# Kernel optimization log

Hardware: AMD Instinct MI355X
Metric: run time of the kernel (lower is better)

Reference implementation:

```python
import jax, jax.numpy as jnp
import numpy as np

D_MODEL = 1024
D_INNER = 4096
K = 127
B, L = 2, 4096

def setup_inputs() -> dict:
    key = jax.random.key(0)
    k1, k2, k3, k4, k5 = jax.random.split(key, 5)
    x = jax.random.normal(k1, (B, L, D_MODEL), dtype=jnp.float32)
    # in_proj: Linear(d, 2*m) -> weight [2m, d] (torch convention)
    w_in = jax.random.normal(k2, (2 * D_INNER, D_MODEL), dtype=jnp.float32) * (1.0 / np.sqrt(D_MODEL))
    # depthwise conv weight: [m, 1, k] in torch; store as [m, k]
    w_dw = jax.random.normal(k3, (D_INNER, K), dtype=jnp.float32) * (1.0 / np.sqrt(K))
    b_dw = jax.random.normal(k4, (D_INNER,), dtype=jnp.float32) * 0.01
    # out_proj: Linear(m, d) -> weight [d, m]
    w_out = jax.random.normal(k5, (D_MODEL, D_INNER), dtype=jnp.float32) * (1.0 / np.sqrt(D_INNER))
    return {"x": x, "w_in": w_in, "w_dw": w_dw, "b_dw": b_dw, "w_out": w_out}

def _causal_dwconv(v, w_dw, b_dw):
    # v: [B, L, m]; causal depthwise conv with kernel K
    # pad K-1 on the left only (equivalent to torch pad=K-1 then [..., :L])
    v_bcl = jnp.transpose(v, (0, 2, 1))  # [B, m, L]
    out = jax.lax.conv_general_dilated(
        v_bcl,
        w_dw[:, None, :],  # [m, 1, K]
        window_strides=(1,),
        padding=[(K - 1, 0)],
        feature_group_count=D_INNER,
        dimension_numbers=("NCH", "OIH", "NCH"),
    )
    out = out + b_dw[None, :, None]
    return jnp.transpose(out, (0, 2, 1))  # [B, L, m]

def reference(x, w_in, w_dw, b_dw, w_out):
    vg = jnp.einsum("bld,ed->ble", x, w_in)  # [B, L, 2m]
    v, g = jnp.split(vg, 2, axis=-1)
    v = _causal_dwconv(v, w_dw, b_dw)
    y = jax.nn.silu(v) * jax.nn.silu(g)
    return jnp.einsum("blm,dm->bld", y, w_out)
```

## Files before the change

### kernel.cpp

```cpp
#include <hip/hip_runtime.h>
#include <hip/hip_bf16.h>
#include <cstdint>
#include <cstddef>

typedef __fp16 f16_t;
typedef __attribute__((ext_vector_type(8))) __fp16 f16x8;
typedef __attribute__((ext_vector_type(4))) __fp16 f16x4;
typedef __attribute__((ext_vector_type(2))) __fp16 h2_t;
typedef __attribute__((ext_vector_type(4))) float floatx4;

__device__ __forceinline__ void async_copy_16B(const void* g, void* l) {
  __builtin_amdgcn_global_load_lds(
      (const __attribute__((address_space(1))) void*)g,
      (__attribute__((address_space(3))) void*)l, 16, 0, 0);
}

#define ISSUE_FENCE asm volatile("" ::: "memory")

__global__ __launch_bounds__(256) void prep(
    const float* __restrict__ x, const float* __restrict__ w_in,
    const float* __restrict__ w_out, const float* __restrict__ w_dw,
    f16_t* __restrict__ x_h, f16_t* __restrict__ wi_h,
    f16_t* __restrict__ wo_h, h2_t* __restrict__ wp) {
  const int tid = blockIdx.x * 256 + threadIdx.x;
  if (tid < 5242880) {
    const float* src;
    f16_t* dst;
    int off;
    if (tid < 2097152) {
      src = x; dst = x_h; off = tid;
    } else if (tid < 4194304) {
      src = w_in; dst = wi_h; off = tid - 2097152;
    } else {
      src = w_out; dst = wo_h; off = tid - 4194304;
    }
    const float4 v = *(const float4*)(src + (size_t)off * 4);
    f16x4 o;
    o.x = (f16_t)v.x; o.y = (f16_t)v.y; o.z = (f16_t)v.z; o.w = (f16_t)v.w;
    *(f16x4*)(dst + (size_t)off * 4) = o;
  } else {
    const int idx = tid - 5242880;
    if (idx < 128 * 4096) {
      const int p = idx >> 12;
      const int c = idx & 4095;
      float a, b;
      if (p < 126) {
        a = w_dw[c * 127 + p]; b = w_dw[c * 127 + p + 1];
      } else if (p == 126) {
        a = w_dw[c * 127 + 126]; b = 0.f;
      } else {
        a = 0.f; b = w_dw[c * 127 + 0];
      }
      h2_t w;
      w.x = (f16_t)a; w.y = (f16_t)b;
      wp[idx] = w;
    }
  }
}

__global__ __launch_bounds__(512, 2) void gemm256_8p(
    const f16_t* __restrict__ A, const f16_t* __restrict__ B,
    f16_t* __restrict__ C, int M, int N, int K) {
  extern __shared__ char smem[];
  const int t = threadIdx.x;
  const int lane = t & 63;
  const int wave = t >> 6;
  const int wm = wave >> 2;
  const int wn = wave & 3;

  const int bid = blockIdx.x;
  const int swz = (bid & 7) * 128 + (bid >> 3);
  const int m0 = (swz >> 5) * 256;
  const int n0 = (swz & 31) * 256;

  const int fr = lane & 15;
  const int ks = lane >> 4;

  auto stageB = [&](int d, int k0, int half) {
#pragma unroll
    for (int l = 0; l < 2; ++l) {
      const int q = l * 512 + t;
      const int row = half * 128 + (q >> 3);
      const int slot = q & 7;
      const int col = (slot ^ (row & 7)) * 8;
      async_copy_16B(B + (size_t)(n0 + row) * K + k0 + col,
                     smem + d * 65536 + 32768 + row * 128 + slot * 16);
    }
  };
  auto stageA = [&](int d, int k0, int j) {
    const int blk = t >> 8;
    const int row = j * 32 + blk * 128 + ((t & 255) >> 3);
    const int slot = t & 7;
    const int col = (slot ^ (row & 7)) * 8;
    async_copy_16B(A + (size_t)(m0 + row) * K + k0 + col,
                   smem + d * 65536 + row * 128 + slot * 16);
  };
  auto ldA = [&](int d, int R, int kslot) -> f16x8 {
    return *(const f16x8*)(smem + d * 65536 + R * 128 +
                           ((kslot ^ (R & 7)) << 4));
  };
  auto ldB = [&](int d, int R, int kslot) -> f16x8 {
    return *(const f16x8*)(smem + d * 65536 + 32768 + R * 128 +
                           ((kslot ^ (R & 7)) << 4));
  };

  floatx4 acc[8][4] = {};
  const int kTiles = K / 64;

  stageB(0, 0, 0); ISSUE_FENCE;
  stageB(0, 0, 1); ISSUE_FENCE;
  stageA(0, 0, 0); ISSUE_FENCE;
  stageA(0, 0, 1); ISSUE_FENCE;
  stageA(0, 0, 2); ISSUE_FENCE;
  stageA(0, 0, 3); ISSUE_FENCE;
  asm volatile("s_waitcnt vmcnt(3)" ::: "memory");
  __builtin_amdgcn_s_barrier();

  f16x8 bf[4][2];
  for (int tt = 0; tt < kTiles; ++tt) {
    const int d = tt & 1;
    const int kn = (tt + 1) * 64;
    const bool pf = (tt + 1 < kTiles);
#pragma unroll
    for (int q = 0; q < 4; ++q) {
      f16x8 af[2][2];
#pragma unroll
      for (int kh = 0; kh < 2; ++kh) {
#pragma unroll
        for (int ii = 0; ii < 2; ++ii)
          af[ii][kh] = ldA(d, wm * 128 + q * 32 + ii * 16 + fr, kh * 4 + ks);
        if (q == 0)
#pragma unroll
          for (int j = 0; j < 4; ++j)
            bf[j][kh] = ldB(d, wn * 64 + j * 16 + fr, kh * 4 + ks);
      }
      if (pf) {
        if (q == 0) stageB(d ^ 1, kn, 0);
        else if (q == 1) stageB(d ^ 1, kn, 1);
        else if (q == 2) { stageA(d ^ 1, kn, 0); stageA(d ^ 1, kn, 1); }
        else { stageA(d ^ 1, kn, 2); stageA(d ^ 1, kn, 3); }
      }
      if (pf) {
        if (q == 0)      asm volatile("s_waitcnt vmcnt(4)" ::: "memory");
        else if (q == 1) asm volatile("s_waitcnt vmcnt(5)" ::: "memory");
        else if (q == 2) asm volatile("s_waitcnt vmcnt(6)" ::: "memory");
        else             asm volatile("s_waitcnt vmcnt(3)" ::: "memory");
      } else {
        if (q == 0)      asm volatile("s_waitcnt vmcnt(2)" ::: "memory");
        else if (q == 1) asm volatile("s_waitcnt vmcnt(1)" ::: "memory");
        else if (q == 2) asm volatile("s_waitcnt vmcnt(0)" ::: "memory");
      }
      __builtin_amdgcn_s_barrier();
      __builtin_amdgcn_s_setprio(1);
#pragma unroll
      for (int kh = 0; kh < 2; ++kh)
#pragma unroll
        for (int ii = 0; ii < 2; ++ii)
#pragma unroll
          for (int j = 0; j < 4; ++j)
            acc[q * 2 + ii][j] = __builtin_amdgcn_mfma_f32_16x16x32_f16(
                af[ii][kh], bf[j][kh], acc[q * 2 + ii][j], 0, 0, 0);
      __builtin_amdgcn_s_setprio(0);
      __builtin_amdgcn_s_barrier();
    }
  }

  const int cr = (lane >> 4) * 4;
  const int cc = lane & 15;
#pragma unroll
  for (int i = 0; i < 8; ++i)
#pragma unroll
    for (int j = 0; j < 4; ++j)
#pragma unroll
      for (int r = 0; r < 4; ++r) {
        const int row = m0 + wm * 128 + i * 16 + cr + r;
        const int col = n0 + wn * 64 + j * 16 + cc;
        C[(size_t)row * N + col] = (f16_t)acc[i][j][r];
      }
}

__global__ __launch_bounds__(256) void gemm_bt_k128(
    const f16_t* __restrict__ A, const f16_t* __restrict__ B,
    float* __restrict__ C, int M, int N, int K) {
  constexpr int BM_ = 128, BN_ = 64, KP = 4;
  constexpr int NA = BM_ * 4 * KP;
  constexpr int NTOT = (BM_ + BN_) * 4 * KP;
  constexpr int CPT = NTOT / 256;

  __shared__ f16_t smem[(BM_ + BN_) * 128];
  const int t = threadIdx.x;
  const int lane = t & 63;
  const int wave = t >> 6;
  const int m0 = blockIdx.y * BM_;
  const int n0 = blockIdx.x * BN_;
  const int wr = wave * 32;
  const int fr = lane & 15;
  const int fk = (lane >> 4) * 8;

  floatx4 acc[2][4] = {};

  const int kTiles = K / 128;
  for (int kt = 0; kt < kTiles; ++kt) {
    const int k0 = kt * 128;
    __syncthreads();
#pragma unroll
    for (int it = 0; it < CPT; ++it) {
      const int p = it * 256 + t;
      const f16_t* gsrc;
      if (p < NA) {
        const int h = p >> 9;
        const int r = (p >> 2) & (BM_ - 1);
        const int kc = h * 32 + (p & 3) * 8;
        gsrc = A + (size_t)(m0 + r) * K + k0 + kc;
      } else {
        const int q = p - NA;
        const int h = q >> 8;
        const int r = (q >> 2) & (BN_ - 1);
        const int kc = h * 32 + (q & 3) * 8;
        gsrc = B + (size_t)(n0 + r) * K + k0 + kc;
      }
      async_copy_16B(gsrc, smem + p * 8);
    }
    __syncthreads();

#pragma unroll
    for (int h = 0; h < KP; ++h) {
      f16x8 af[2], bf[4];
#pragma unroll
      for (int i = 0; i < 2; ++i)
        af[i] = *(const f16x8*)(smem + h * BM_ * 32 + (wr + i * 16 + fr) * 32 + fk);
#pragma unroll
      for (int j = 0; j < 4; ++j)
        bf[j] = *(const f16x8*)(smem + NA * 8 + h * BN_ * 32 + (j * 16 + fr) * 32 + fk);
#pragma unroll
      for (int i = 0; i < 2; ++i)
#pragma unroll
        for (int j = 0; j < 4; ++j)
          acc[i][j] = __builtin_amdgcn_mfma_f32_16x16x32_f16(
              af[i], bf[j], acc[i][j], 0, 0, 0);
    }
  }

  const int cr = (lane >> 4) * 4;
  const int cc = lane & 15;
#pragma unroll
  for (int i = 0; i < 2; ++i)
#pragma unroll
    for (int j = 0; j < 4; ++j)
#pragma unroll
      for (int r = 0; r < 4; ++r) {
        const int row = m0 + wr + i * 16 + cr + r;
        const int col = n0 + j * 16 + cc;
        C[(size_t)row * N + col] = acc[i][j][r];
      }
}

#define CONV_L 128
#define CPAIRS 127

__global__ __launch_bounds__(256) void conv_gate(
    const f16_t* __restrict__ vg, const h2_t* __restrict__ wp,
    const float* __restrict__ b_dw, f16_t* __restrict__ y) {
  __shared__ uint32_t vtp[CPAIRS * 64];
  __shared__ uint32_t wpl[128 * 64];
  const int t = threadIdx.x;
  const int lane = t & 63;
  const int wave = t >> 6;
  const int c0 = blockIdx.x * 64;
  const int lt = blockIdx.y & 31;
  const int b = blockIdx.y >> 5;
  const int l0 = lt * CONV_L;

#pragma unroll
  for (int it = 0; it < 8; ++it) {
    const int q = it * 256 + t;
    async_copy_16B(wp + (size_t)(q >> 4) * 4096 + c0 + (q & 15) * 4,
                   wpl + q * 4);
  }
  for (int q = t; q < CPAIRS * 8; q += 256) {
    const int m = q >> 3;
    const int oc = (q & 7) * 8;
    const int le = l0 - 126 + 2 * m;
    uint4 a = make_uint4(0u, 0u, 0u, 0u);
    uint4 bb = make_uint4(0u, 0u, 0u, 0u);
    if (le >= 0) {
      const size_t base = (size_t)(b * 4096 + le) * 8192 + c0 + oc;
      a = *(const uint4*)(vg + base);
      bb = *(const uint4*)(vg + base + 8192);
    }
    uint32_t* dst = vtp + m * 64 + oc;
    const uint32_t aw[4] = {a.x, a.y, a.z, a.w};
    const uint32_t bw[4] = {bb.x, bb.y, bb.z, bb.w};
#pragma unroll
    for (int i = 0; i < 4; ++i) {
      dst[2 * i] = (aw[i] & 0xFFFFu) | (bw[i] << 16);
      dst[2 * i + 1] = (aw[i] >> 16) | (bw[i] & 0xFFFF0000u);
    }
  }

  const int c = c0 + lane;
  const int lb = l0 + wave * 32;
  const f16_t* gp = vg + (size_t)(b * 4096 + lb) * 8192 + 4096 + c;
  f16_t gvals[32];
#pragma unroll
  for (int i = 0; i < 32; ++i) gvals[i] = gp[(size_t)i * 8192];

  __syncthreads();

  const float bias = b_dw[c];
  float acc[32];
#pragma unroll
  for (int i = 0; i < 32; ++i) acc[i] = bias;

  const uint32_t* vbase = vtp + wave * 16 * 64 + lane;
  const uint32_t* wbase = wpl + lane;

  h2_t ring[17];
#pragma unroll
  for (int m = 0; m < 17; ++m)
    ring[m] = __builtin_bit_cast(h2_t, vbase[m * 64]);

  {
    const h2_t w0 = __builtin_bit_cast(h2_t, wbase[127 * 64]);
#pragma unroll
    for (int h = 0; h < 16; ++h)
      acc[2 * h + 1] =
          __builtin_amdgcn_fdot2(w0, ring[h], acc[2 * h + 1], false);
  }

#pragma unroll
  for (int k = 0; k < 64; ++k) {
    const h2_t we = __builtin_bit_cast(h2_t, wbase[(2 * k) * 64]);
#pragma unroll
    for (int h = 0; h < 16; ++h)
      acc[2 * h] =
          __builtin_amdgcn_fdot2(we, ring[(k + h) % 17], acc[2 * h], false);
    if (k < 63) {
      const h2_t wo = __builtin_bit_cast(h2_t, wbase[(2 * k + 1) * 64]);
#pragma unroll
      for (int h = 0; h < 16; ++h)
        acc[2 * h + 1] = __builtin_amdgcn_fdot2(wo, ring[(k + 1 + h) % 17],
                                                acc[2 * h + 1], false);
      if (k < 62)
        ring[k % 17] = __builtin_bit_cast(h2_t, vbase[(17 + k) * 64]);
    }
  }

  f16_t* yp = y + (size_t)(b * 4096 + lb) * 4096 + c;
#pragma unroll
  for (int i = 0; i < 32; ++i) {
    const float gv = (float)gvals[i];
    const float v = acc[i];
    const float sv = v / (1.f + __expf(-v));
    const float sg = gv / (1.f + __expf(-gv));
    yp[(size_t)i * 4096] = (f16_t)(sv * sg);
  }
}

extern "C" void kernel_launch(void* const* d_in, const int* in_sizes, int n_in,
                              void* d_out, int out_size, void* d_ws,
                              size_t ws_size, hipStream_t stream) {
  const float* x     = (const float*)d_in[0];
  const float* w_in  = (const float*)d_in[1];
  const float* w_dw  = (const float*)d_in[2];
  const float* b_dw  = (const float*)d_in[3];
  const float* w_out = (const float*)d_in[4];
  float* out = (float*)d_out;

  char* p = (char*)d_ws;
  f16_t* x_h  = (f16_t*)p; p += (size_t)8192 * 1024 * 2;
  f16_t* wi_h = (f16_t*)p; p += (size_t)8192 * 1024 * 2;
  f16_t* wo_h = (f16_t*)p; p += (size_t)1024 * 4096 * 2;
  h2_t*  wp   = (h2_t*)p;  p += (size_t)128 * 4096 * 4;
  f16_t* vg   = (f16_t*)p; p += (size_t)8192 * 8192 * 2;
  f16_t* y    = (f16_t*)p; p += (size_t)8192 * 4096 * 2;

  prep<<<22528, 256, 0, stream>>>(x, w_in, w_out, w_dw, x_h, wi_h, wo_h, wp);

  hipFuncSetAttribute(reinterpret_cast<const void*>(gemm256_8p),
                      hipFuncAttributeMaxDynamicSharedMemorySize, 131072);
  gemm256_8p<<<1024, 512, 131072, stream>>>(x_h, wi_h, vg, 8192, 8192, 1024);

  conv_gate<<<dim3(64, 64), 256, 0, stream>>>(vg, wp, b_dw, y);
  gemm_bt_k128<<<dim3(16, 64), 256, 0, stream>>>(y, wo_h, out,
                                                 8192, 1024, 4096);
}
```

Baseline: 502.6 us.

## Deepen GEMM prefetch to two tiles ahead and remap blocks per XCD

```diff
diff --git a/kernel.cpp b/kernel.cpp
--- a/kernel.cpp
+++ b/kernel.cpp
@@ -14,8 +14,6 @@
       (const __attribute__((address_space(1))) void*)g,
       (__attribute__((address_space(3))) void*)l, 16, 0, 0);
 }
-
-#define ISSUE_FENCE asm volatile("" ::: "memory")
 
 __global__ __launch_bounds__(256) void prep(
     const float* __restrict__ x, const float* __restrict__ w_in,
@@ -69,17 +67,21 @@
   const int wn = wave & 3;
 
   const int bid = blockIdx.x;
-  const int swz = (bid & 7) * 128 + (bid >> 3);
-  const int m0 = (swz >> 5) * 256;
-  const int n0 = (swz & 31) * 256;
+  const int xcd = bid & 7;
+  const int l = bid >> 3;
+  const int quad = l >> 5;
+  const int qm = (l >> 3) & 3;
+  const int qn = l & 7;
+  const int m0 = ((xcd >> 1) * 8 + (quad >> 1) * 4 + qm) * 256;
+  const int n0 = ((xcd & 1) * 16 + (quad & 1) * 8 + qn) * 256;
 
   const int fr = lane & 15;
   const int ks = lane >> 4;
 
   auto stageB = [&](int d, int k0, int half) {
 #pragma unroll
-    for (int l = 0; l < 2; ++l) {
-      const int q = l * 512 + t;
+    for (int u = 0; u < 2; ++u) {
+      const int q = u * 512 + t;
       const int row = half * 128 + (q >> 3);
       const int slot = q & 7;
       const int col = (slot ^ (row & 7)) * 8;
@@ -107,20 +109,21 @@
   floatx4 acc[8][4] = {};
   const int kTiles = K / 64;
 
-  stageB(0, 0, 0); ISSUE_FENCE;
-  stageB(0, 0, 1); ISSUE_FENCE;
-  stageA(0, 0, 0); ISSUE_FENCE;
-  stageA(0, 0, 1); ISSUE_FENCE;
-  stageA(0, 0, 2); ISSUE_FENCE;
-  stageA(0, 0, 3); ISSUE_FENCE;
-  asm volatile("s_waitcnt vmcnt(3)" ::: "memory");
+  stageB(0, 0, 0); stageB(0, 0, 1);
+  stageA(0, 0, 0); stageA(0, 0, 1); stageA(0, 0, 2); stageA(0, 0, 3);
+  stageB(1, 64, 0); stageA(1, 64, 0);
+  stageB(1, 64, 1); stageA(1, 64, 1);
+  stageA(1, 64, 2);
+  asm volatile("s_waitcnt vmcnt(7)" ::: "memory");
   __builtin_amdgcn_s_barrier();
 
   f16x8 bf[4][2];
   for (int tt = 0; tt < kTiles; ++tt) {
     const int d = tt & 1;
-    const int kn = (tt + 1) * 64;
-    const bool pf = (tt + 1 < kTiles);
+    const int k1 = (tt + 1) * 64;
+    const int k2 = (tt + 2) * 64;
+    const bool pf1 = (tt + 1 < kTiles);
+    const bool pf2 = (tt + 2 < kTiles);
 #pragma unroll
     for (int q = 0; q < 4; ++q) {
       f16x8 af[2][2];
@@ -134,23 +137,22 @@
           for (int j = 0; j < 4; ++j)
             bf[j][kh] = ldB(d, wn * 64 + j * 16 + fr, kh * 4 + ks);
       }
-      if (pf) {
-        if (q == 0) stageB(d ^ 1, kn, 0);
-        else if (q == 1) stageB(d ^ 1, kn, 1);
-        else if (q == 2) { stageA(d ^ 1, kn, 0); stageA(d ^ 1, kn, 1); }
-        else { stageA(d ^ 1, kn, 2); stageA(d ^ 1, kn, 3); }
-      }
-      if (pf) {
-        if (q == 0)      asm volatile("s_waitcnt vmcnt(4)" ::: "memory");
-        else if (q == 1) asm volatile("s_waitcnt vmcnt(5)" ::: "memory");
-        else if (q == 2) asm volatile("s_waitcnt vmcnt(6)" ::: "memory");
-        else             asm volatile("s_waitcnt vmcnt(3)" ::: "memory");
+      if (q == 0) {
+        if (pf1) stageA(d ^ 1, k1, 3);
+      } else if (q == 1) {
+        if (pf2) { stageB(d, k2, 0); stageA(d, k2, 0); }
+      } else if (q == 2) {
+        if (pf2) { stageB(d, k2, 1); stageA(d, k2, 1); }
       } else {
-        if (q == 0)      asm volatile("s_waitcnt vmcnt(2)" ::: "memory");
-        else if (q == 1) asm volatile("s_waitcnt vmcnt(1)" ::: "memory");
-        else if (q == 2) asm volatile("s_waitcnt vmcnt(0)" ::: "memory");
+        if (pf2) {
+          stageA(d, k2, 2);
+          asm volatile("s_waitcnt vmcnt(7)" ::: "memory");
+        } else if (pf1) {
+          asm volatile("s_waitcnt vmcnt(0)" ::: "memory");
+        }
       }
       __builtin_amdgcn_s_barrier();
+      asm volatile("s_waitcnt lgkmcnt(0)" ::: "memory");
       __builtin_amdgcn_s_setprio(1);
 #pragma unroll
       for (int kh = 0; kh < 2; ++kh)
```

Result: no change. 495.0 us (-1.5%).
